# Performance work log

Measured on AMD Instinct MI355X. Metric: run time of the kernel, lower is better.

## Reference

```python
import jax, jax.numpy as jnp
import numpy as np
from jax import lax

B, S, L = 32768, 3, 5
D1, D2, OUT = 32, 64, 541
EPS = 1e-5


def setup_inputs() -> dict:
    key = jax.random.key(0)
    ks = jax.random.split(key, 8)
    inp = {
        "x": jax.random.normal(ks[0], (B, S, L), dtype=jnp.float32),
        "w1": jax.random.normal(ks[1], (S, D1, 1, 3), dtype=jnp.float32) * 0.2,
        "b1": jax.random.normal(ks[2], (S, D1), dtype=jnp.float32) * 0.1,
        "w2": jax.random.normal(ks[3], (S, D2, D1, 3), dtype=jnp.float32) * 0.1,
        "b2": jax.random.normal(ks[4], (S, D2), dtype=jnp.float32) * 0.1,
        "gamma": jnp.ones((S, D2), dtype=jnp.float32),
        "beta": jnp.zeros((S, D2), dtype=jnp.float32),
        "wl": jax.random.normal(ks[5], (S, OUT, D2 * L), dtype=jnp.float32) * 0.05,
        "bl": jax.random.normal(ks[6], (S, OUT), dtype=jnp.float32) * 0.05,
    }
    return inp


def _conv1d(h, w):
    # h: [B, Cin, L], w: [Cout, Cin, 3], padding=1 (same)
    return lax.conv_general_dilated(h, w, window_strides=(1,), padding=((1, 1),),
                                    dimension_numbers=("NCH", "OIH", "NCH"))


def _subnet(xi, w1, b1, w2, b2, g, be, wl, bl):
    # xi: [B, L] -> [B, 1, L]
    h = _conv1d(xi[:, None, :], w1) + b1[None, :, None]          # [B, D1, L]
    h = jax.nn.gelu(h, approximate=False)
    h = _conv1d(h, w2) + b2[None, :, None]                        # [B, D2, L]
    h = jax.nn.gelu(h, approximate=False)
    # BatchNorm1d (training mode): per-channel stats over (batch, length), biased var
    mean = jnp.mean(h, axis=(0, 2), keepdims=True)
    var = jnp.mean(jnp.square(h - mean), axis=(0, 2), keepdims=True)
    h = (h - mean) * lax.rsqrt(var + EPS) * g[None, :, None] + be[None, :, None]
    h = h.reshape(h.shape[0], -1)                                 # flatten [B, D2*L]
    return h @ wl.T + bl                                          # [B, OUT]


def reference(x, w1, b1, w2, b2, gamma, beta, wl, bl):
    xs = jnp.moveaxis(x, 1, 0)  # [S, B, L]
    outs = jax.vmap(_subnet)(xs, w1, b1, w2, b2, gamma, beta, wl, bl)  # [S, B, OUT]
    return jnp.moveaxis(outs, 0, 1)  # [B, S, OUT]
```

## Files before the change

kernel.cpp:

```cpp
#include <hip/hip_runtime.h>
#include <hip/hip_bf16.h>

#define B_ 32768
#define S_ 3
#define L_ 5
#define D1 32
#define D2 64
#define OUT_N 541
#define OUT_PAD 576
#define KDIM 320
#define EPS_ 1e-5f

typedef __attribute__((ext_vector_type(8))) short bf16x8;
typedef __attribute__((ext_vector_type(4))) float f32x4;

__device__ __forceinline__ short f2bf(float f) {
    __hip_bfloat16 h = __float2bfloat16(f);
    return *reinterpret_cast<short*>(&h);
}
__device__ __forceinline__ float bf2f(short u) {
    union { float f; unsigned v; } x;
    x.v = ((unsigned)(unsigned short)u) << 16;
    return x.f;
}

__device__ __forceinline__ float gelu_fast(float x) {
    float x2 = x * x;
    float u = x * fmaf(x2, -0.0713548162726f, -1.59576912161f);
    float e = __expf(u);
    float r = __builtin_amdgcn_rcpf(1.0f + e);
    return x * r;
}

__device__ __forceinline__ void cp16(void* lds, const void* g) {
    __builtin_amdgcn_global_load_lds(
        (const __attribute__((address_space(1))) unsigned int*)g,
        (__attribute__((address_space(3))) unsigned int*)lds, 16, 0, 0);
}

__global__ __launch_bounds__(256, 3) void k_feat(
    const float* __restrict__ x, const float* __restrict__ w1, const float* __restrict__ b1,
    const float* __restrict__ w2, const float* __restrict__ b2,
    __hip_bfloat16* __restrict__ H, float* __restrict__ stats)
{
    const int s   = blockIdx.y;
    const int tid = threadIdx.x;
    const int ci  = tid & 7;
    const int bi  = tid >> 3;
    const int b   = blockIdx.x * 32 + bi;

    __shared__ __align__(16) float sw1[D1 * 3];
    __shared__ float sb1[D1];
    __shared__ __align__(16) float sw2T[D1 * 3 * D2];
    __shared__ float sb2[D2];
    __shared__ __align__(16) short sh1[32 * 264];
    __shared__ float sred[4][8][16];

    float xv[L_ + 2];
    xv[0] = 0.f; xv[L_ + 1] = 0.f;
    const float* xp = x + (size_t)b * (S_ * L_) + s * L_;
#pragma unroll
    for (int l = 0; l < L_; ++l) xv[l + 1] = xp[l];

    for (int i = tid; i < D1 * 3; i += 256) sw1[i] = w1[s * D1 * 3 + i];
    for (int i = tid; i < D1; i += 256)     sb1[i] = b1[s * D1 + i];
    for (int i = tid; i < D2; i += 256)     sb2[i] = b2[s * D2 + i];
    for (int i = tid; i < D1 * 3 * D2; i += 256) {
        int c2 = i & 63, t = i >> 6;
        int dl = t % 3, c1 = t / 3;
        sw2T[i] = w2[((size_t)(s * D2 + c2) * D1 + c1) * 3 + dl];
    }
    __syncthreads();

#pragma unroll
    for (int k = 0; k < 4; ++k) {
        const int c1 = ci * 4 + k;
        const float wa = sw1[c1 * 3 + 0], wb = sw1[c1 * 3 + 1], wc = sw1[c1 * 3 + 2];
        const float bb = sb1[c1];
        bf16x8 pk;
#pragma unroll
        for (int l = 0; l < L_; ++l) {
            float v = fmaf(wa, xv[l], fmaf(wb, xv[l + 1], fmaf(wc, xv[l + 2], bb)));
            pk[l] = f2bf(gelu_fast(v));
        }
        pk[5] = 0; pk[6] = 0; pk[7] = 0;
        *(bf16x8*)&sh1[bi * 264 + c1 * 8] = pk;
    }
    __syncthreads();

    float acc[8][5];
#pragma unroll
    for (int j = 0; j < 8; ++j) {
        const float bb = sb2[ci * 8 + j];
#pragma unroll
        for (int l = 0; l < 5; ++l) acc[j][l] = bb;
    }

#pragma unroll 2
    for (int c1 = 0; c1 < D1; ++c1) {
        bf16x8 hv = *(const bf16x8*)&sh1[bi * 264 + c1 * 8];
        const float p0 = bf2f(hv[0]), p1 = bf2f(hv[1]), p2 = bf2f(hv[2]),
                    p3 = bf2f(hv[3]), p4 = bf2f(hv[4]);
        const float* wbase = &sw2T[c1 * 3 * 64 + ci * 8];
        f32x4 w0a = *(const f32x4*)(wbase + 0 * 64);
        f32x4 w0b = *(const f32x4*)(wbase + 0 * 64 + 4);
        f32x4 w1a = *(const f32x4*)(wbase + 1 * 64);
        f32x4 w1b = *(const f32x4*)(wbase + 1 * 64 + 4);
        f32x4 w2a = *(const f32x4*)(wbase + 2 * 64);
        f32x4 w2b = *(const f32x4*)(wbase + 2 * 64 + 4);
#pragma unroll
        for (int j = 0; j < 8; ++j) {
            const float wA = (j < 4) ? w0a[j & 3] : w0b[j & 3];
            const float wB = (j < 4) ? w1a[j & 3] : w1b[j & 3];
            const float wC = (j < 4) ? w2a[j & 3] : w2b[j & 3];
            acc[j][0] = fmaf(wB, p0, fmaf(wC, p1, acc[j][0]));
            acc[j][1] = fmaf(wA, p0, fmaf(wB, p1, fmaf(wC, p2, acc[j][1])));
            acc[j][2] = fmaf(wA, p1, fmaf(wB, p2, fmaf(wC, p3, acc[j][2])));
            acc[j][3] = fmaf(wA, p2, fmaf(wB, p3, fmaf(wC, p4, acc[j][3])));
            acc[j][4] = fmaf(wA, p3, fmaf(wB, p4, acc[j][4]));
        }
    }

    bf16x8 hbv[5];
    float su[8], sq[8];
#pragma unroll
    for (int j = 0; j < 8; ++j) { su[j] = 0.f; sq[j] = 0.f; }
#pragma unroll
    for (int t = 0; t < 5; ++t) {
#pragma unroll
        for (int e = 0; e < 8; ++e) {
            const int idx = t * 8 + e;
            const int j = idx / 5, l = idx % 5;
            float g = gelu_fast(acc[j][l]);
            short hb = f2bf(g);
            hbv[t][e] = hb;
            float gq = bf2f(hb);
            su[j] += gq;
            sq[j] = fmaf(gq, gq, sq[j]);
        }
    }
    bf16x8* dst = (bf16x8*)(H + ((size_t)s * B_ + b) * KDIM + ci * 40);
#pragma unroll
    for (int t = 0; t < 5; ++t) dst[t] = hbv[t];

#pragma unroll
    for (int j = 0; j < 8; ++j) {
        su[j] += __shfl_down(su[j], 32); sq[j] += __shfl_down(sq[j], 32);
        su[j] += __shfl_down(su[j], 16); sq[j] += __shfl_down(sq[j], 16);
        su[j] += __shfl_down(su[j], 8);  sq[j] += __shfl_down(sq[j], 8);
    }
    const int wid = tid >> 6;
    const int lane = tid & 63;
    if (lane < 8) {
#pragma unroll
        for (int j = 0; j < 8; ++j) {
            sred[wid][lane][j] = su[j];
            sred[wid][lane][8 + j] = sq[j];
        }
    }
    __syncthreads();
    if (tid < 128) {
        const int which = tid >> 6;
        const int c2 = tid & 63;
        const int rci = c2 >> 3, rj = c2 & 7;
        float v = sred[0][rci][which * 8 + rj] + sred[1][rci][which * 8 + rj]
                + sred[2][rci][which * 8 + rj] + sred[3][rci][which * 8 + rj];
        atomicAdd(&stats[(s * D2 + c2) * 2 + which], v);
    }
}

__global__ void k_stats(const float* __restrict__ stats,
                        const float* __restrict__ gamma, const float* __restrict__ beta,
                        float* __restrict__ af, float* __restrict__ cf)
{
    int i = threadIdx.x;
    if (i < S_ * D2) {
        const float n = (float)B_ * (float)L_;
        float su = stats[i * 2 + 0], sq = stats[i * 2 + 1];
        float mean = su / n;
        float var = sq / n - mean * mean;
        float rstd = rsqrtf(var + EPS_);
        float a = gamma[i] * rstd;
        af[i] = a;
        cf[i] = beta[i] - mean * a;
    }
}

__global__ __launch_bounds__(64) void k_fold(
    const float* __restrict__ wl, const float* __restrict__ bl,
    const float* __restrict__ af, const float* __restrict__ cf,
    __hip_bfloat16* __restrict__ Wp, float* __restrict__ blp)
{
    const int row = blockIdx.x;
    const int s = row / OUT_PAD, o = row % OUT_PAD;
    const int lane = threadIdx.x;
    short* Wb = (short*)Wp + (size_t)s * 40 * 576 * 8;

    if (o >= OUT_N) {
#pragma unroll
        for (int t = 0; t < 5; ++t) {
            const int k = lane * 5 + t;
            const int idx = (((k >> 5) * 4 + ((k >> 3) & 3)) * 576 + o) * 8 + (k & 7);
            Wb[idx] = f2bf(0.f);
        }
        if (lane == 0) blp[row] = 0.f;
        return;
    }
    const float* wsrc = wl + ((size_t)s * OUT_N + o) * KDIM;
    const float a = af[s * D2 + lane];
    const float c = cf[s * D2 + lane];
    float bacc = 0.f;
#pragma unroll
    for (int t = 0; t < 5; ++t) {
        const int k = lane * 5 + t;
        float wv = wsrc[k];
        const int idx = (((k >> 5) * 4 + ((k >> 3) & 3)) * 576 + o) * 8 + (k & 7);
        Wb[idx] = f2bf(wv * a);
        bacc = fmaf(wv, c, bacc);
    }
#pragma unroll
    for (int off = 32; off > 0; off >>= 1) bacc += __shfl_down(bacc, off);
    if (lane == 0) blp[row] = bacc + bl[s * OUT_N + o];
}

__global__ __launch_bounds__(256, 3) void k_gemm(
    const __hip_bfloat16* __restrict__ H, const __hip_bfloat16* __restrict__ Wp,
    const float* __restrict__ blp, float* __restrict__ out)
{
    const int s    = blockIdx.z;
    const int bm   = blockIdx.x * 32;
    const int tid  = threadIdx.x;
    const int wave = tid >> 6;
    const int lane = tid & 63;
    const int lm   = lane & 15;
    const int quad = lane >> 4;

    __shared__ __align__(16) short sA[32 * 320];

    const short* Hs = (const short*)H + (size_t)s * B_ * KDIM;

#pragma unroll
    for (int i = 0; i < 5; ++i) {
        const int f = i * 256 + tid;
        const int row = f / 40, cslot = f % 40;
        const int cg = (cslot & ~7) | ((cslot & 7) ^ (row & 7));
        cp16(&sA[f * 8], Hs + (size_t)(bm + row) * KDIM + cg * 8);
    }
    __syncthreads();

    const short* Bs = (const short*)Wp + (size_t)s * 40 * 576 * 8;
    const int colw = wave * 144;

    f32x4 acc[2][9];
#pragma unroll
    for (int mt = 0; mt < 2; ++mt)
#pragma unroll
        for (int nt = 0; nt < 9; ++nt) acc[mt][nt] = (f32x4){0.f, 0.f, 0.f, 0.f};

#pragma unroll
    for (int ks = 0; ks < 10; ++ks) {
        bf16x8 bfr[9];
#pragma unroll
        for (int nt = 0; nt < 9; ++nt) {
            bfr[nt] = *(const bf16x8*)(Bs +
                ((size_t)(ks * 4 + quad) * 576 + colw + nt * 16 + lm) * 8);
        }
#pragma unroll
        for (int mt = 0; mt < 2; ++mt) {
            const int row = mt * 16 + lm;
            const int chunk = ks * 4 + quad;
            const int swz = (chunk & ~7) | ((chunk & 7) ^ (row & 7));
            bf16x8 af = *(const bf16x8*)&sA[row * 320 + swz * 8];
#pragma unroll
            for (int nt = 0; nt < 9; ++nt)
                acc[mt][nt] = __builtin_amdgcn_mfma_f32_16x16x32_bf16(
                    af, bfr[nt], acc[mt][nt], 0, 0, 0);
        }
    }

    float bias[9];
#pragma unroll
    for (int nt = 0; nt < 9; ++nt) bias[nt] = blp[s * OUT_PAD + colw + nt * 16 + lm];

#pragma unroll
    for (int mt = 0; mt < 2; ++mt) {
#pragma unroll
        for (int r = 0; r < 4; ++r) {
            const int row = bm + mt * 16 + quad * 4 + r;
            float* orow = out + ((size_t)row * S_ + s) * OUT_N;
#pragma unroll
            for (int nt = 0; nt < 9; ++nt) {
                const int col = colw + nt * 16 + lm;
                if (col < OUT_N) orow[col] = acc[mt][nt][r] + bias[nt];
            }
        }
    }
}

extern "C" void kernel_launch(void* const* d_in, const int* in_sizes, int n_in,
                              void* d_out, int out_size, void* d_ws, size_t ws_size,
                              hipStream_t stream) {
    const float* x     = (const float*)d_in[0];
    const float* w1    = (const float*)d_in[1];
    const float* b1    = (const float*)d_in[2];
    const float* w2    = (const float*)d_in[3];
    const float* b2    = (const float*)d_in[4];
    const float* gamma = (const float*)d_in[5];
    const float* beta  = (const float*)d_in[6];
    const float* wl    = (const float*)d_in[7];
    const float* bl    = (const float*)d_in[8];
    float* out = (float*)d_out;

    char* ws = (char*)d_ws;
    __hip_bfloat16* H = (__hip_bfloat16*)ws;
    size_t offH = (size_t)S_ * B_ * KDIM * sizeof(__hip_bfloat16);
    float* stats = (float*)(ws + offH);
    float* af = stats + S_ * D2 * 2;
    float* cf = af + S_ * D2;
    __hip_bfloat16* Wp = (__hip_bfloat16*)(cf + S_ * D2);
    float* blp = (float*)((char*)Wp + (size_t)S_ * OUT_PAD * KDIM * sizeof(__hip_bfloat16));

    hipMemsetAsync(stats, 0, (size_t)S_ * D2 * 2 * sizeof(float), stream);

    k_feat<<<dim3(B_ / 32, S_), 256, 0, stream>>>(x, w1, b1, w2, b2, H, stats);
    k_stats<<<1, 256, 0, stream>>>(stats, gamma, beta, af, cf);
    k_fold<<<S_ * OUT_PAD, 64, 0, stream>>>(wl, bl, af, cf, Wp, blp);
    k_gemm<<<dim3(B_ / 32, 1, S_), 256, 0, stream>>>(H, Wp, blp, out);
}
```

Before: 441.7 us.

## Compute second conv layer with bf16 MFMA instead of scalar FMAs

Replaces the per-thread scalar FP32 FMA loop for the second convolution with 16x16x32 bf16 MFMA instructions. Layer-1 activations are stored position-major with zero padding, and w2 is packed as bf16 B fragments per tap. Results go through a new LDS staging buffer so the existing GELU-output, stats and store code can read them back in the old layout. Weights are now rounded to bf16, which lowers precision, and the kernel gains an extra barrier and more LDS traffic.

```diff
diff --git a/kernel.cpp b/kernel.cpp
--- a/kernel.cpp
+++ b/kernel.cpp
@@ -12,6 +12,7 @@
 #define EPS_ 1e-5f
 
 typedef __attribute__((ext_vector_type(8))) short bf16x8;
+typedef __attribute__((ext_vector_type(4))) short bf16x4;
 typedef __attribute__((ext_vector_type(4))) float f32x4;
 
 __device__ __forceinline__ short f2bf(float f) {
@@ -49,11 +50,16 @@
     const int bi  = tid >> 3;
     const int b   = blockIdx.x * 32 + bi;
 
-    __shared__ __align__(16) float sw1[D1 * 3];
+    const int wave = tid >> 6;
+    const int lane = tid & 63;
+    const int lm   = lane & 15;
+    const int quad = lane >> 4;
+
+    __shared__ __align__(16) short sh1T[32 * 232];
+    __shared__ __align__(16) short sw2B[3 * 64 * 32];
+    __shared__ __align__(16) short sh2[32 * 328];
+    __shared__ float sw1[D1 * 3];
     __shared__ float sb1[D1];
-    __shared__ __align__(16) float sw2T[D1 * 3 * D2];
-    __shared__ float sb2[D2];
-    __shared__ __align__(16) short sh1[32 * 264];
     __shared__ float sred[4][8][16];
 
     float xv[L_ + 2];
@@ -62,64 +68,69 @@
 #pragma unroll
     for (int l = 0; l < L_; ++l) xv[l + 1] = xp[l];
 
+    const float bc = b2[s * D2 + wave * 16 + lm];
+
     for (int i = tid; i < D1 * 3; i += 256) sw1[i] = w1[s * D1 * 3 + i];
     for (int i = tid; i < D1; i += 256)     sb1[i] = b1[s * D1 + i];
-    for (int i = tid; i < D2; i += 256)     sb2[i] = b2[s * D2 + i];
     for (int i = tid; i < D1 * 3 * D2; i += 256) {
-        int c2 = i & 63, t = i >> 6;
-        int dl = t % 3, c1 = t / 3;
-        sw2T[i] = w2[((size_t)(s * D2 + c2) * D1 + c1) * 3 + dl];
-    }
-    __syncthreads();
-
+        const int dl = i % 3, t = i / 3;
+        sw2B[dl * 2048 + t] = f2bf(w2[s * D1 * 3 * D2 + i]);
+    }
+    __syncthreads();
+
+    float wk0[4], wk1[4], wk2[4], bk[4];
 #pragma unroll
     for (int k = 0; k < 4; ++k) {
         const int c1 = ci * 4 + k;
-        const float wa = sw1[c1 * 3 + 0], wb = sw1[c1 * 3 + 1], wc = sw1[c1 * 3 + 2];
-        const float bb = sb1[c1];
-        bf16x8 pk;
-#pragma unroll
-        for (int l = 0; l < L_; ++l) {
-            float v = fmaf(wa, xv[l], fmaf(wb, xv[l + 1], fmaf(wc, xv[l + 2], bb)));
-            pk[l] = f2bf(gelu_fast(v));
-        }
-        pk[5] = 0; pk[6] = 0; pk[7] = 0;
-        *(bf16x8*)&sh1[bi * 264 + c1 * 8] = pk;
-    }
-    __syncthreads();
-
-    float acc[8][5];
-#pragma unroll
-    for (int j = 0; j < 8; ++j) {
-        const float bb = sb2[ci * 8 + j];
-#pragma unroll
-        for (int l = 0; l < 5; ++l) acc[j][l] = bb;
-    }
-
-#pragma unroll 2
-    for (int c1 = 0; c1 < D1; ++c1) {
-        bf16x8 hv = *(const bf16x8*)&sh1[bi * 264 + c1 * 8];
-        const float p0 = bf2f(hv[0]), p1 = bf2f(hv[1]), p2 = bf2f(hv[2]),
-                    p3 = bf2f(hv[3]), p4 = bf2f(hv[4]);
-        const float* wbase = &sw2T[c1 * 3 * 64 + ci * 8];
-        f32x4 w0a = *(const f32x4*)(wbase + 0 * 64);
-        f32x4 w0b = *(const f32x4*)(wbase + 0 * 64 + 4);
-        f32x4 w1a = *(const f32x4*)(wbase + 1 * 64);
-        f32x4 w1b = *(const f32x4*)(wbase + 1 * 64 + 4);
-        f32x4 w2a = *(const f32x4*)(wbase + 2 * 64);
-        f32x4 w2b = *(const f32x4*)(wbase + 2 * 64 + 4);
-#pragma unroll
-        for (int j = 0; j < 8; ++j) {
-            const float wA = (j < 4) ? w0a[j & 3] : w0b[j & 3];
-            const float wB = (j < 4) ? w1a[j & 3] : w1b[j & 3];
-            const float wC = (j < 4) ? w2a[j & 3] : w2b[j & 3];
-            acc[j][0] = fmaf(wB, p0, fmaf(wC, p1, acc[j][0]));
-            acc[j][1] = fmaf(wA, p0, fmaf(wB, p1, fmaf(wC, p2, acc[j][1])));
-            acc[j][2] = fmaf(wA, p1, fmaf(wB, p2, fmaf(wC, p3, acc[j][2])));
-            acc[j][3] = fmaf(wA, p2, fmaf(wB, p3, fmaf(wC, p4, acc[j][3])));
-            acc[j][4] = fmaf(wA, p3, fmaf(wB, p4, acc[j][4]));
-        }
-    }
+        wk0[k] = sw1[c1 * 3 + 0]; wk1[k] = sw1[c1 * 3 + 1]; wk2[k] = sw1[c1 * 3 + 2];
+        bk[k] = sb1[c1];
+    }
+    const bf16x4 z4 = (bf16x4){0, 0, 0, 0};
+    *(bf16x4*)&sh1T[bi * 232 + 0 * 32 + ci * 4] = z4;
+    *(bf16x4*)&sh1T[bi * 232 + 6 * 32 + ci * 4] = z4;
+#pragma unroll
+    for (int l = 0; l < L_; ++l) {
+        bf16x4 pk;
+#pragma unroll
+        for (int k = 0; k < 4; ++k) {
+            float v = fmaf(wk0[k], xv[l], fmaf(wk1[k], xv[l + 1], fmaf(wk2[k], xv[l + 2], bk[k])));
+            pk[k] = f2bf(gelu_fast(v));
+        }
+        *(bf16x4*)&sh1T[bi * 232 + (l + 1) * 32 + ci * 4] = pk;
+    }
+    __syncthreads();
+
+    bf16x8 bfr[3];
+#pragma unroll
+    for (int dl = 0; dl < 3; ++dl)
+        bfr[dl] = *(const bf16x8*)&sw2B[dl * 2048 + (wave * 16 + lm) * 32 + quad * 8];
+
+    f32x4 acc[10];
+#pragma unroll
+    for (int mt = 0; mt < 10; ++mt) acc[mt] = (f32x4){bc, bc, bc, bc};
+
+#pragma unroll
+    for (int mt = 0; mt < 10; ++mt) {
+        const int l  = mt >> 1;
+        const int bb = (mt & 1) * 16 + lm;
+#pragma unroll
+        for (int dl = 0; dl < 3; ++dl) {
+            bf16x8 af = *(const bf16x8*)&sh1T[bb * 232 + (l + dl) * 32 + quad * 8];
+            acc[mt] = __builtin_amdgcn_mfma_f32_16x16x32_bf16(af, bfr[dl], acc[mt], 0, 0, 0);
+        }
+    }
+
+    const int c2w = wave * 16 + lm;
+#pragma unroll
+    for (int mt = 0; mt < 10; ++mt) {
+        const int l = mt >> 1;
+#pragma unroll
+        for (int r = 0; r < 4; ++r) {
+            const int bb = (mt & 1) * 16 + quad * 4 + r;
+            sh2[bb * 328 + c2w * 5 + l] = f2bf(gelu_fast(acc[mt][r]));
+        }
+    }
+    __syncthreads();
 
     bf16x8 hbv[5];
     float su[8], sq[8];
@@ -127,14 +138,12 @@
     for (int j = 0; j < 8; ++j) { su[j] = 0.f; sq[j] = 0.f; }
 #pragma unroll
     for (int t = 0; t < 5; ++t) {
+        hbv[t] = *(const bf16x8*)&sh2[bi * 328 + ci * 40 + t * 8];
 #pragma unroll
         for (int e = 0; e < 8; ++e) {
             const int idx = t * 8 + e;
-            const int j = idx / 5, l = idx % 5;
-            float g = gelu_fast(acc[j][l]);
-            short hb = f2bf(g);
-            hbv[t][e] = hb;
-            float gq = bf2f(hb);
+            const int j = idx / 5;
+            float gq = bf2f(hbv[t][e]);
             su[j] += gq;
             sq[j] = fmaf(gq, gq, sq[j]);
         }
@@ -150,7 +159,6 @@
         su[j] += __shfl_down(su[j], 8);  sq[j] += __shfl_down(sq[j], 8);
     }
     const int wid = tid >> 6;
-    const int lane = tid & 63;
     if (lane < 8) {
 #pragma unroll
         for (int j = 0; j < 8; ++j) {
```

Measured after the change: 413.5 us. 1.07x faster.
